# Optimization experiments

Measured on AMD Instinct MI355X. Metric: run time of the kernel, lower is better.

## Reference

```python
import jax, jax.numpy as jnp
import numpy as np
from collections import deque

N = 768          # number of nodes (x.shape[0])
DEG = 8          # out-degree of the random directed graph
E = N * DEG      # number of edges
H = 32           # head_num
MAX_ENTRIES = 10_000_000  # fixed COO size (pad with zero coeff)
MAX_PATHS = 3    # original truncates all_shortest_paths to first 3


def _build_graph_coeffs():
    """Replicates the networkx all_shortest_paths logic exactly, emitting a
    flat COO list: out[i,j] += coeff * enc[node] with
    coeff = 1 / (len(path) * num_paths_ij), num_paths_ij <= 3."""
    rng = np.random.default_rng(0)
    src = rng.integers(0, N, E)
    dst = rng.integers(0, N, E)
    adj = [[] for _ in range(N)]
    for u, v in zip(src.tolist(), dst.tolist()):
        if u != v:  # self-loops never appear on a shortest path
            adj[u].append(v)
    pair_l, node_l, coeff_l = [], [], []
    for i in range(N):
        # BFS from i, recording shortest-path predecessor DAG
        dist = [-1] * N
        pred = [None] * N
        dist[i] = 0
        q = deque([i])
        while q:
            u = q.popleft()
            du1 = dist[u] + 1
            for v in adj[u]:
                if dist[v] == -1:
                    dist[v] = du1
                    pred[v] = [u]
                    q.append(v)
                elif dist[v] == du1:
                    pred[v].append(u)
        base = i * N
        for j in range(N):
            if dist[j] == -1:
                continue  # unreachable -> out[i,j] stays 0 (the `except: continue`)
            # enumerate up to MAX_PATHS shortest paths via predecessor DAG
            paths = []
            stack = [(j, (j,))]
            while stack and len(paths) < MAX_PATHS:
                v, path = stack.pop()
                if v == i:
                    paths.append(path)
                    continue
                for u in pred[v]:
                    stack.append((u, path + (u,)))
            k = len(paths)
            pij = base + j
            for path in paths:
                c = 1.0 / (len(path) * k)  # per-path node mean, then mean over paths
                for n in path:
                    pair_l.append(pij)
                    node_l.append(n)
                    coeff_l.append(c)
    pair = np.asarray(pair_l, dtype=np.int32)
    node = np.asarray(node_l, dtype=np.int32)
    coeff = np.asarray(coeff_l, dtype=np.float32)
    m = pair.shape[0]
    if m > MAX_ENTRIES:
        pair, node, coeff = pair[:MAX_ENTRIES], node[:MAX_ENTRIES], coeff[:MAX_ENTRIES]
    else:
        pad = MAX_ENTRIES - m
        pair = np.concatenate([pair, np.zeros(pad, np.int32)])
        node = np.concatenate([node, np.zeros(pad, np.int32)])
        coeff = np.concatenate([coeff, np.zeros(pad, np.float32)])
    return src, dst, pair, node, coeff


def setup_inputs() -> dict:
    key = jax.random.key(0)
    k1, k2, k3, k4 = jax.random.split(key, 4)
    src, dst, pair, node, coeff = _build_graph_coeffs()
    bound = 1.0 / np.sqrt(4.0)  # nn.Linear(4, H) default init range
    return {
        "x": jax.random.normal(k1, (N, 128), jnp.float32),
        "edge_attr": jax.random.normal(k2, (N, 4), jnp.float32),
        "W": jax.random.uniform(k3, (H, 4), jnp.float32, -bound, bound),
        "b": jax.random.uniform(k4, (H,), jnp.float32, -bound, bound),
        "edge_idx": jnp.asarray(np.stack([src, dst]).astype(np.int64)),
        "pair_idx": jnp.asarray(pair),
        "node_idx": jnp.asarray(node),
        "coeff": jnp.asarray(coeff),
        "num_nodes": N,
    }


def reference(x, edge_attr, W, b, edge_idx, pair_idx, node_idx, coeff, num_nodes):
    n = num_nodes
    enc = edge_attr @ W.T + b                      # [N, H] edge_encoder per node
    vals = coeff[:, None] * enc[node_idx]          # [M, H] weighted gather
    out = jax.ops.segment_sum(vals, pair_idx, num_segments=n * n)  # [N*N, H]
    return out.reshape(n, n, -1).transpose(2, 0, 1)  # 'h w n -> n h w'
```

## Files before the change

kernel.cpp:

```cpp
#include <hip/hip_runtime.h>

#define N2 (768 * 768)
#define NH 32
#define PPB 256
#define CHUNKS 3
#define CAP 6144

__global__ __launch_bounds__(256) void fused_kernel(
    const int* __restrict__ pair, const int* __restrict__ node,
    const float* __restrict__ coeff, const float* __restrict__ ea,
    const float* __restrict__ W, const float* __restrict__ b,
    float* __restrict__ out, int M)
{
    __shared__ float2 ent[CAP];
    __shared__ int ps[PPB], pe[PPB];
    __shared__ int sBnd[CHUNKS + 1];
    __shared__ float sW[NH * 4];
    __shared__ float sBias[NH];

    const int t = threadIdx.x;
    const int pbase = blockIdx.x * (PPB * CHUNKS);

    if (t < NH * 4) sW[t] = W[t];
    if (t < NH) sBias[t] = b[t];

    if (t <= CHUNKS) {
        int target = pbase + t * PPB;
        int lo = 0, hi = M;
        while (lo < hi) {
            int mid = (lo + hi) >> 1;
            int key = (coeff[mid] == 0.f) ? 0x7fffffff : pair[mid];
            if (key < target) lo = mid + 1; else hi = mid;
        }
        sBnd[t] = lo;
    }

    for (int c = 0; c < CHUNKS; ++c) {
        __syncthreads();
        ps[t] = 0; pe[t] = 0;
        __syncthreads();
        const int p0 = pbase + c * PPB;
        const int s0 = sBnd[c], s1 = sBnd[c + 1];
        const int cnt = s1 - s0;
        float a0 = 0.f, a1 = 0.f, a2 = 0.f, a3 = 0.f, a4 = 0.f;

        if (cnt <= CAP) {
            for (int i = t; i < cnt; i += PPB) {
                int e = s0 + i;
                float cc = coeff[e];
                int nd = node[e];
                ent[i] = make_float2(cc, __int_as_float(nd));
                int pp = pair[e];
                if (i == 0 || pair[e - 1] != pp) ps[pp - p0] = i;
                if (i == cnt - 1 || pair[e + 1] != pp) pe[pp - p0] = i + 1;
            }
            __syncthreads();
            const int s = ps[t], e = pe[t];
            for (int k = s; k < e; ++k) {
                float2 en = ent[k];
                float cc = en.x;
                int nd = __float_as_int(en.y);
                const float4 v = *reinterpret_cast<const float4*>(ea + nd * 4);
                a0 += cc;
                a1 += cc * v.x; a2 += cc * v.y; a3 += cc * v.z; a4 += cc * v.w;
            }
        } else {
            __syncthreads();
            const int tgt = p0 + t;
            int lo = s0, hi = s1;
            while (lo < hi) { int mid = (lo + hi) >> 1; if (pair[mid] < tgt) lo = mid + 1; else hi = mid; }
            const int s = lo; hi = s1;
            while (lo < hi) { int mid = (lo + hi) >> 1; if (pair[mid] <= tgt) lo = mid + 1; else hi = mid; }
            for (int k = s; k < lo; ++k) {
                float cc = coeff[k];
                const float4 v = *reinterpret_cast<const float4*>(ea + node[k] * 4);
                a0 += cc;
                a1 += cc * v.x; a2 += cc * v.y; a3 += cc * v.z; a4 += cc * v.w;
            }
        }

        const size_t op = (size_t)p0 + t;
#pragma unroll
        for (int h = 0; h < NH; ++h) {
            out[(size_t)h * N2 + op] =
                sBias[h] * a0 + sW[h * 4 + 0] * a1 + sW[h * 4 + 1] * a2
              + sW[h * 4 + 2] * a3 + sW[h * 4 + 3] * a4;
        }
    }
}

extern "C" void kernel_launch(void* const* d_in, const int* in_sizes, int n_in,
                              void* d_out, int out_size, void* d_ws, size_t ws_size,
                              hipStream_t stream) {
    const float* ea    = (const float*)d_in[1];
    const float* W     = (const float*)d_in[2];
    const float* b     = (const float*)d_in[3];
    const int*   pair  = (const int*)d_in[5];
    const int*   node  = (const int*)d_in[6];
    const float* coeff = (const float*)d_in[7];
    float* out = (float*)d_out;
    int M = in_sizes[5];

    fused_kernel<<<N2 / (PPB * CHUNKS), PPB, 0, stream>>>(
        pair, node, coeff, ea, W, b, out, M);
}
```

Before: 57.78 us.

## Split each pair across four lanes with shuffle reduction and nontemporal stores

Restructures the fused gather/segment-sum kernel so each block handles 64 pairs per chunk, with four threads cooperating on every pair and combining partial sums via xor shuffles. The large shared-memory entry staging buffer and the binary-search fallback are removed, and entries are read directly from global memory. Output is written by all 256 threads, each covering 8 heads of a pair, using nontemporal stores. This raises block count and occupancy by cutting shared memory use and evens out per-pair work, at the cost of more blocks, more syncs and up-front binary searches per block.

```diff
diff --git a/kernel.cpp b/kernel.cpp
--- a/kernel.cpp
+++ b/kernel.cpp
@@ -2,9 +2,9 @@
 
 #define N2 (768 * 768)
 #define NH 32
-#define PPB 256
-#define CHUNKS 3
-#define CAP 6144
+#define PPC 64
+#define CHUNKS 4
+#define TPB 256
 
 __global__ __launch_bounds__(256) void fused_kernel(
     const int* __restrict__ pair, const int* __restrict__ node,
@@ -12,20 +12,20 @@
     const float* __restrict__ W, const float* __restrict__ b,
     float* __restrict__ out, int M)
 {
-    __shared__ float2 ent[CAP];
-    __shared__ int ps[PPB], pe[PPB];
+    __shared__ int ps[PPC], pe[PPC];
+    __shared__ float sum[5][PPC];
     __shared__ int sBnd[CHUNKS + 1];
     __shared__ float sW[NH * 4];
     __shared__ float sBias[NH];
 
     const int t = threadIdx.x;
-    const int pbase = blockIdx.x * (PPB * CHUNKS);
+    const int pbase = blockIdx.x * (PPC * CHUNKS);
 
     if (t < NH * 4) sW[t] = W[t];
     if (t < NH) sBias[t] = b[t];
 
     if (t <= CHUNKS) {
-        int target = pbase + t * PPB;
+        int target = pbase + t * PPC;
         int lo = 0, hi = M;
         while (lo < hi) {
             int mid = (lo + hi) >> 1;
@@ -34,58 +34,64 @@
         }
         sBnd[t] = lo;
     }
+    __syncthreads();
 
     for (int c = 0; c < CHUNKS; ++c) {
+        if (t < PPC) { ps[t] = 0; pe[t] = 0; }
         __syncthreads();
-        ps[t] = 0; pe[t] = 0;
-        __syncthreads();
-        const int p0 = pbase + c * PPB;
+        const int p0 = pbase + c * PPC;
         const int s0 = sBnd[c], s1 = sBnd[c + 1];
         const int cnt = s1 - s0;
-        float a0 = 0.f, a1 = 0.f, a2 = 0.f, a3 = 0.f, a4 = 0.f;
 
-        if (cnt <= CAP) {
-            for (int i = t; i < cnt; i += PPB) {
-                int e = s0 + i;
-                float cc = coeff[e];
-                int nd = node[e];
-                ent[i] = make_float2(cc, __int_as_float(nd));
-                int pp = pair[e];
-                if (i == 0 || pair[e - 1] != pp) ps[pp - p0] = i;
-                if (i == cnt - 1 || pair[e + 1] != pp) pe[pp - p0] = i + 1;
-            }
-            __syncthreads();
-            const int s = ps[t], e = pe[t];
-            for (int k = s; k < e; ++k) {
-                float2 en = ent[k];
-                float cc = en.x;
-                int nd = __float_as_int(en.y);
+        for (int i = t; i < cnt; i += TPB) {
+            int e = s0 + i;
+            int pp = pair[e];
+            if (i == 0 || pair[e - 1] != pp) ps[pp - p0] = i;
+            if (i == cnt - 1 || pair[e + 1] != pp) pe[pp - p0] = i + 1;
+        }
+        __syncthreads();
+
+        {
+            const int q = t >> 2, sub = t & 3;
+            float a0 = 0.f, a1 = 0.f, a2 = 0.f, a3 = 0.f, a4 = 0.f;
+            const int ke = s0 + pe[q];
+            for (int k = s0 + ps[q] + sub; k < ke; k += 4) {
+                float cc = coeff[k];
+                int nd = node[k];
                 const float4 v = *reinterpret_cast<const float4*>(ea + nd * 4);
                 a0 += cc;
                 a1 += cc * v.x; a2 += cc * v.y; a3 += cc * v.z; a4 += cc * v.w;
             }
-        } else {
-            __syncthreads();
-            const int tgt = p0 + t;
-            int lo = s0, hi = s1;
-            while (lo < hi) { int mid = (lo + hi) >> 1; if (pair[mid] < tgt) lo = mid + 1; else hi = mid; }
-            const int s = lo; hi = s1;
-            while (lo < hi) { int mid = (lo + hi) >> 1; if (pair[mid] <= tgt) lo = mid + 1; else hi = mid; }
-            for (int k = s; k < lo; ++k) {
-                float cc = coeff[k];
-                const float4 v = *reinterpret_cast<const float4*>(ea + node[k] * 4);
-                a0 += cc;
-                a1 += cc * v.x; a2 += cc * v.y; a3 += cc * v.z; a4 += cc * v.w;
+#pragma unroll
+            for (int d = 1; d < 4; d <<= 1) {
+                a0 += __shfl_xor(a0, d);
+                a1 += __shfl_xor(a1, d);
+                a2 += __shfl_xor(a2, d);
+                a3 += __shfl_xor(a3, d);
+                a4 += __shfl_xor(a4, d);
+            }
+            if (sub == 0) {
+                sum[0][q] = a0; sum[1][q] = a1; sum[2][q] = a2;
+                sum[3][q] = a3; sum[4][q] = a4;
             }
         }
+        __syncthreads();
 
-        const size_t op = (size_t)p0 + t;
+        {
+            const int q2 = t & 63;
+            const int cb = t >> 6;
+            const float a0 = sum[0][q2], a1 = sum[1][q2], a2 = sum[2][q2],
+                        a3 = sum[3][q2], a4 = sum[4][q2];
+            const size_t op = (size_t)(p0 + q2);
 #pragma unroll
-        for (int h = 0; h < NH; ++h) {
-            out[(size_t)h * N2 + op] =
-                sBias[h] * a0 + sW[h * 4 + 0] * a1 + sW[h * 4 + 1] * a2
-              + sW[h * 4 + 2] * a3 + sW[h * 4 + 3] * a4;
+            for (int j = 0; j < 8; ++j) {
+                const int h = cb * 8 + j;
+                float val = sBias[h] * a0 + sW[h * 4 + 0] * a1 + sW[h * 4 + 1] * a2
+                          + sW[h * 4 + 2] * a3 + sW[h * 4 + 3] * a4;
+                __builtin_nontemporal_store(val, out + (size_t)h * N2 + op);
+            }
         }
+        __syncthreads();
     }
 }
 
@@ -101,6 +107,6 @@
     float* out = (float*)d_out;
     int M = in_sizes[5];
 
-    fused_kernel<<<N2 / (PPB * CHUNKS), PPB, 0, stream>>>(
+    fused_kernel<<<N2 / (PPC * CHUNKS), TPB, 0, stream>>>(
         pair, node, coeff, ea, W, b, out, M);
 }
```

Result: slower. 65.72 us (+13.7%).

## Drop shared-memory entry staging, one chunk per block, dual-accumulator gather loop

Applied to the files above, without the earlier changes.

Each block now handles a single 256-pair chunk instead of three, giving three times as many blocks. The 48KB shared staging buffer for coeff/node entries is removed, along with the binary-search fallback path. Threads now read coeff and node straight from global memory using absolute segment bounds, and the gather loop is unrolled by two with separate accumulators. This is meant to raise occupancy and memory-level parallelism, at the cost of more boundary binary searches and uncoalesced per-thread global reads instead of coalesced staging.

```diff
diff --git a/kernel.cpp b/kernel.cpp
--- a/kernel.cpp
+++ b/kernel.cpp
@@ -3,29 +3,26 @@
 #define N2 (768 * 768)
 #define NH 32
 #define PPB 256
-#define CHUNKS 3
-#define CAP 6144
+#define TPB 256
 
 __global__ __launch_bounds__(256) void fused_kernel(
     const int* __restrict__ pair, const int* __restrict__ node,
     const float* __restrict__ coeff, const float* __restrict__ ea,
-    const float* __restrict__ W, const float* __restrict__ b,
+    const float* __restrict__ W, const float* __restrict__ bias,
     float* __restrict__ out, int M)
 {
-    __shared__ float2 ent[CAP];
     __shared__ int ps[PPB], pe[PPB];
-    __shared__ int sBnd[CHUNKS + 1];
+    __shared__ int sBnd[2];
     __shared__ float sW[NH * 4];
     __shared__ float sBias[NH];
 
     const int t = threadIdx.x;
-    const int pbase = blockIdx.x * (PPB * CHUNKS);
+    const int p0 = blockIdx.x * PPB;
 
     if (t < NH * 4) sW[t] = W[t];
-    if (t < NH) sBias[t] = b[t];
-
-    if (t <= CHUNKS) {
-        int target = pbase + t * PPB;
+    if (t < NH) sBias[t] = bias[t];
+    if (t < 2) {
+        int target = p0 + t * PPB;
         int lo = 0, hi = M;
         while (lo < hi) {
             int mid = (lo + hi) >> 1;
@@ -34,58 +31,50 @@
         }
         sBnd[t] = lo;
     }
+    ps[t] = 0; pe[t] = 0;
+    __syncthreads();
 
-    for (int c = 0; c < CHUNKS; ++c) {
-        __syncthreads();
-        ps[t] = 0; pe[t] = 0;
-        __syncthreads();
-        const int p0 = pbase + c * PPB;
-        const int s0 = sBnd[c], s1 = sBnd[c + 1];
-        const int cnt = s1 - s0;
-        float a0 = 0.f, a1 = 0.f, a2 = 0.f, a3 = 0.f, a4 = 0.f;
+    const int s0 = sBnd[0], s1 = sBnd[1];
+    const int cnt = s1 - s0;
 
-        if (cnt <= CAP) {
-            for (int i = t; i < cnt; i += PPB) {
-                int e = s0 + i;
-                float cc = coeff[e];
-                int nd = node[e];
-                ent[i] = make_float2(cc, __int_as_float(nd));
-                int pp = pair[e];
-                if (i == 0 || pair[e - 1] != pp) ps[pp - p0] = i;
-                if (i == cnt - 1 || pair[e + 1] != pp) pe[pp - p0] = i + 1;
-            }
-            __syncthreads();
-            const int s = ps[t], e = pe[t];
-            for (int k = s; k < e; ++k) {
-                float2 en = ent[k];
-                float cc = en.x;
-                int nd = __float_as_int(en.y);
-                const float4 v = *reinterpret_cast<const float4*>(ea + nd * 4);
-                a0 += cc;
-                a1 += cc * v.x; a2 += cc * v.y; a3 += cc * v.z; a4 += cc * v.w;
-            }
-        } else {
-            __syncthreads();
-            const int tgt = p0 + t;
-            int lo = s0, hi = s1;
-            while (lo < hi) { int mid = (lo + hi) >> 1; if (pair[mid] < tgt) lo = mid + 1; else hi = mid; }
-            const int s = lo; hi = s1;
-            while (lo < hi) { int mid = (lo + hi) >> 1; if (pair[mid] <= tgt) lo = mid + 1; else hi = mid; }
-            for (int k = s; k < lo; ++k) {
-                float cc = coeff[k];
-                const float4 v = *reinterpret_cast<const float4*>(ea + node[k] * 4);
-                a0 += cc;
-                a1 += cc * v.x; a2 += cc * v.y; a3 += cc * v.z; a4 += cc * v.w;
-            }
+    for (int i = t; i < cnt; i += TPB) {
+        int e = s0 + i;
+        int pp = pair[e];
+        if (i == 0 || pair[e - 1] != pp) ps[pp - p0] = e;
+        if (i == cnt - 1 || pair[e + 1] != pp) pe[pp - p0] = e + 1;
+    }
+    __syncthreads();
+
+    float a0 = 0.f, a1 = 0.f, a2 = 0.f, a3 = 0.f, a4 = 0.f;
+    {
+        int k = ps[t];
+        const int e = pe[t];
+        float b0 = 0.f, b1 = 0.f, b2 = 0.f, b3 = 0.f, b4 = 0.f;
+        for (; k + 2 <= e; k += 2) {
+            const float cA = coeff[k],     cB = coeff[k + 1];
+            const int   nA = node[k],      nB = node[k + 1];
+            const float4 vA = *reinterpret_cast<const float4*>(ea + nA * 4);
+            const float4 vB = *reinterpret_cast<const float4*>(ea + nB * 4);
+            a0 += cA;        b0 += cB;
+            a1 += cA * vA.x; b1 += cB * vB.x;
+            a2 += cA * vA.y; b2 += cB * vB.y;
+            a3 += cA * vA.z; b3 += cB * vB.z;
+            a4 += cA * vA.w; b4 += cB * vB.w;
         }
+        if (k < e) {
+            const float cA = coeff[k];
+            const float4 vA = *reinterpret_cast<const float4*>(ea + node[k] * 4);
+            a0 += cA; a1 += cA * vA.x; a2 += cA * vA.y; a3 += cA * vA.z; a4 += cA * vA.w;
+        }
+        a0 += b0; a1 += b1; a2 += b2; a3 += b3; a4 += b4;
+    }
 
-        const size_t op = (size_t)p0 + t;
+    const size_t op = (size_t)p0 + t;
 #pragma unroll
-        for (int h = 0; h < NH; ++h) {
-            out[(size_t)h * N2 + op] =
-                sBias[h] * a0 + sW[h * 4 + 0] * a1 + sW[h * 4 + 1] * a2
-              + sW[h * 4 + 2] * a3 + sW[h * 4 + 3] * a4;
-        }
+    for (int h = 0; h < NH; ++h) {
+        out[(size_t)h * N2 + op] =
+            sBias[h] * a0 + sW[h * 4 + 0] * a1 + sW[h * 4 + 1] * a2
+          + sW[h * 4 + 2] * a3 + sW[h * 4 + 3] * a4;
     }
 }
 
@@ -101,6 +90,5 @@
     float* out = (float*)d_out;
     int M = in_sizes[5];
 
-    fused_kernel<<<N2 / (PPB * CHUNKS), PPB, 0, stream>>>(
-        pair, node, coeff, ea, W, b, out, M);
+    fused_kernel<<<N2 / PPB, TPB, 0, stream>>>(pair, node, coeff, ea, W, b, out, M);
 }
```

Result: slower. 64.93 us (+12.4%).
